# Kernel optimization log

Hardware: AMD Instinct MI355X
Metric: run time of the kernel (lower is better)

## Reference

```python
import jax, jax.numpy as jnp
import numpy as np

LN_EPS = 1e-5


def setup_inputs() -> dict:
    key = jax.random.key(0)
    k1, k2 = jax.random.split(key, 2)
    B, N, D = 8, 4096, 1024
    Z = jax.random.normal(k1, (B, N, D), dtype=jnp.float32)
    # raw decay parameter (sigmoid is applied in forward, as in the torch module)
    decay = jnp.float32(0.9)
    # nn.Linear(d, d): weight [D, D] (out, in), bias [D]
    W = jax.random.normal(k2, (D, D), dtype=jnp.float32) / np.sqrt(D).astype(np.float32)
    b = jnp.zeros((D,), dtype=jnp.float32)
    # nn.LayerNorm(d): gamma/beta
    gamma = jnp.ones((D,), dtype=jnp.float32)
    beta = jnp.zeros((D,), dtype=jnp.float32)
    return {"Z": Z, "decay": decay, "W": W, "b": b, "gamma": gamma, "beta": beta}


def _ema_scan(Z, a):
    """s_t = a * s_{t-1} + Z_t via O(log N) associative scan over slot axis."""
    B, N, D = Z.shape
    A = jnp.full((B, N, 1), a, dtype=Z.dtype)  # broadcast decay coeff per step

    def combine(x, y):
        a1, b1 = x
        a2, b2 = y
        return (a1 * a2, b1 * a2 + b2)

    _, S = jax.lax.associative_scan(combine, (A, Z), axis=1)
    return S  # [B, N, D]


def reference(Z, decay, W, b, gamma, beta):
    a = jax.nn.sigmoid(decay)
    S = _ema_scan(Z, a)                                  # EMA state per slot
    Y = jnp.einsum('bnd,ed->bne', S, W) + b              # per-step Linear, batched
    mu = jnp.mean(Y, axis=-1, keepdims=True)             # LayerNorm over D
    var = jnp.mean((Y - mu) ** 2, axis=-1, keepdims=True)
    Yn = (Y - mu) * jax.lax.rsqrt(var + LN_EPS)
    return Yn * gamma + beta
```

## Files before the change

kernel.cpp:

```cpp
#include <hip/hip_runtime.h>
#include <hip/hip_bf16.h>
#include <cstdint>
#include <cstddef>

#define NB 8
#define NN 4096
#define ND 1024
#define NM (NB*NN)
#define CH 64
#define NCHK (NN/CH)
#define WU 32
#define LN_EPS 1e-5f

typedef __bf16 bf16x8 __attribute__((ext_vector_type(8)));
typedef float  f32x4  __attribute__((ext_vector_type(4)));

typedef __attribute__((address_space(1))) unsigned int guint;
typedef __attribute__((address_space(3))) unsigned int luint;

__device__ __forceinline__ float sigmoidf_(float x) { return 1.f / (1.f + __expf(-x)); }

__device__ __forceinline__ unsigned short f2bf(float x) {
  __hip_bfloat16 h = __float2bfloat16(x);
  return *reinterpret_cast<unsigned short*>(&h);
}
__device__ __forceinline__ float bf2f(unsigned short u) {
  unsigned int v = ((unsigned int)u) << 16;
  return *reinterpret_cast<float*>(&v);
}

__global__ void scan_conv(const float* __restrict__ Z, const float* __restrict__ decay,
                          unsigned short* __restrict__ Sl,
                          const float* __restrict__ W, unsigned short* __restrict__ Wb) {
  const int bid = (int)blockIdx.x;
  if (bid >= NB * NCHK) {
    const int i = (bid - NB * NCHK) * 256 + (int)threadIdx.x;
    float4 v = reinterpret_cast<const float4*>(W)[i];
    ushort4 o;
    o.x = f2bf(v.x); o.y = f2bf(v.y); o.z = f2bf(v.z); o.w = f2bf(v.w);
    reinterpret_cast<ushort4*>(Wb)[i] = o;
    return;
  }
  const float a = sigmoidf_(decay[0]);
  const int c  = bid & (NCHK - 1);
  const int d4 = (int)threadIdx.x;
  const float4* zc = reinterpret_cast<const float4*>(Z + (size_t)bid * CH * ND) + d4;
  ushort4* so = reinterpret_cast<ushort4*>(Sl + (size_t)bid * CH * ND) + d4;
  float4 s = {0.f, 0.f, 0.f, 0.f};
  if (c != 0) {
    const float4* zw = zc - (size_t)WU * (ND / 4);
#pragma unroll 4
    for (int j = 0; j < WU; ++j) {
      float4 v = zw[(size_t)j * (ND / 4)];
      s.x = fmaf(a, s.x, v.x);
      s.y = fmaf(a, s.y, v.y);
      s.z = fmaf(a, s.z, v.z);
      s.w = fmaf(a, s.w, v.w);
    }
  }
#pragma unroll 4
  for (int j = 0; j < CH; ++j) {
    float4 v = zc[(size_t)j * (ND / 4)];
    s.x = fmaf(a, s.x, v.x);
    s.y = fmaf(a, s.y, v.y);
    s.z = fmaf(a, s.z, v.z);
    s.w = fmaf(a, s.w, v.w);
    ushort4 o;
    o.x = f2bf(s.x); o.y = f2bf(s.y); o.z = f2bf(s.z); o.w = f2bf(s.w);
    so[(size_t)j * (ND / 4)] = o;
  }
}

#define BAR()    asm volatile("s_barrier" ::: "memory")
#define LGKM0()  asm volatile("s_waitcnt lgkmcnt(0)" ::: "memory")
#define VM6()    asm volatile("s_waitcnt vmcnt(6)" ::: "memory")
#define VM0()    asm volatile("s_waitcnt vmcnt(0)" ::: "memory")
#define SCHED0() __builtin_amdgcn_sched_barrier(0)
#define PRIO1    __builtin_amdgcn_s_setprio(1)
#define PRIO0    __builtin_amdgcn_s_setprio(0)

#define LOAD_A(qm, D) _Pragma("unroll") for (int i = 0; i < 4; ++i) { \
    aF[i][0] = *(const bf16x8*)(smem + (D)*65536 + aBase + ((qm)*64 + i*16)*128 + swz0); \
    aF[i][1] = *(const bf16x8*)(smem + (D)*65536 + aBase + ((qm)*64 + i*16)*128 + swz1); }

#define LOAD_B(qn, D) _Pragma("unroll") for (int fc = 0; fc < 2; ++fc) { \
    bF[qn][fc][0] = *(const bf16x8*)(smem + (D)*65536 + bBase + ((qn)*32 + fc*16)*128 + swz0); \
    bF[qn][fc][1] = *(const bf16x8*)(smem + (D)*65536 + bBase + ((qn)*32 + fc*16)*128 + swz1); }

#define MFMA_Q(qm, qn) _Pragma("unroll") for (int i = 0; i < 4; ++i) \
    _Pragma("unroll") for (int fc = 0; fc < 2; ++fc) { \
    acc[(qm)*4+i][(qn)*2+fc] = __builtin_amdgcn_mfma_f32_16x16x32_bf16(aF[i][0], bF[qn][fc][0], acc[(qm)*4+i][(qn)*2+fc], 0, 0, 0); \
    acc[(qm)*4+i][(qn)*2+fc] = __builtin_amdgcn_mfma_f32_16x16x32_bf16(aF[i][1], bF[qn][fc][1], acc[(qm)*4+i][(qn)*2+fc], 0, 0, 0); }

#define TILE(t, D, STA, STB, STC, DOVM6, DOVM0) do { \
    LOAD_A(0, D); LOAD_B(0, D); \
    if (STA) stage_h(4*(t)+7); \
    BAR(); LGKM0(); SCHED0(); \
    PRIO1; MFMA_Q(0, 0); PRIO0; SCHED0(); BAR(); \
    LOAD_B(1, D); \
    BAR(); LGKM0(); SCHED0(); \
    PRIO1; MFMA_Q(0, 1); PRIO0; SCHED0(); BAR(); \
    LOAD_A(1, D); \
    if (STB) { stage_h(4*(t)+8); stage_h(4*(t)+9); } \
    BAR(); LGKM0(); SCHED0(); \
    PRIO1; MFMA_Q(1, 0); PRIO0; SCHED0(); BAR(); \
    if (STC) stage_h(4*(t)+10); \
    if (DOVM6) VM6(); \
    if (DOVM0) VM0(); \
    BAR(); \
    PRIO1; MFMA_Q(1, 1); PRIO0; SCHED0(); BAR(); \
  } while (0)

__global__ void __launch_bounds__(512, 2) gemm256(
    const unsigned short* __restrict__ A,
    const unsigned short* __restrict__ Bm,
    const float* __restrict__ bias,
    unsigned short* __restrict__ Yb) {
  extern __shared__ char smem[];
  const int tid  = (int)threadIdx.x;
  const int wid  = tid >> 6, lane = tid & 63;
  const int wr   = wid >> 2, wc = wid & 3;
  const int r16  = lane & 15, kg = lane >> 4;

  const int L = (int)blockIdx.x;
  const int G = (L & 7) * 64 + (L >> 3);
  const int bmAbs = (G >> 2) * 256;
  const int bnAbs = (G & 3) * 256;

  auto stage_h = [&](int h) {
    const int s = h >> 2, j = h & 3;
    const int isB = (j >> 1) ^ 1;
    const int half = j & 1;
    const unsigned short* base = isB ? Bm : A;
    const int rowAbs = (isB ? bnAbs : bmAbs) + half * 128 + wid * 16 + (lane >> 3);
    const int col = s * 64 + (((lane & 7) ^ (lane >> 3)) << 3);
    const int ldsOff = ((s & 1) << 16) + (isB << 15) + (half << 14) + (wid << 11);
    __builtin_amdgcn_global_load_lds((const guint*)(base + (size_t)rowAbs * ND + col),
                                     (luint*)(smem + ldsOff), 16, 0, 0);
    __builtin_amdgcn_global_load_lds((const guint*)(base + (size_t)(rowAbs + 8) * ND + col),
                                     (luint*)(smem + ldsOff + 1024), 16, 0, 0);
  };

  bf16x8 aF[4][2];
  bf16x8 bF[2][2][2];
  f32x4 acc[8][4];
  const f32x4 z4 = {0.f, 0.f, 0.f, 0.f};
#pragma unroll
  for (int m = 0; m < 8; ++m)
#pragma unroll
    for (int n = 0; n < 4; ++n) acc[m][n] = z4;

  const int aBase = (wr << 14) + r16 * 128;
  const int bBase = (1 << 15) + ((wc >> 1) << 14) + (((wc & 1) << 6) + r16) * 128;
  const int swz0 = ((kg)     ^ (lane & 7)) << 4;
  const int swz1 = ((4 + kg) ^ (lane & 7)) << 4;

#pragma unroll
  for (int h = 0; h < 7; ++h) stage_h(h);
  VM6(); BAR();

#pragma unroll 1
  for (int it = 0; it < 7; ++it) {
    TILE(2 * it,     0, 1, 1, 1, 1, 0);
    TILE(2 * it + 1, 1, 1, 1, 1, 1, 0);
  }
  TILE(14, 0, 1, 0, 0, 0, 1);
  TILE(15, 1, 0, 0, 0, 0, 0);

  float bv[4];
#pragma unroll
  for (int n = 0; n < 4; ++n) bv[n] = bias[bnAbs + wc * 64 + n * 16 + r16];
#pragma unroll
  for (int m = 0; m < 8; ++m) {
    const int row0 = wr * 128 + m * 16 + kg * 4;
#pragma unroll
    for (int n = 0; n < 4; ++n) {
      const int col = wc * 64 + n * 16 + r16;
#pragma unroll
      for (int r = 0; r < 4; ++r)
        *reinterpret_cast<unsigned short*>(smem + (row0 + r) * 512 + col * 2) =
            f2bf(acc[m][n][r] + bv[n]);
    }
  }
  __syncthreads();
#pragma unroll
  for (int i = 0; i < 16; ++i) {
    const int idx = i * 512 + tid;
    const int row = idx >> 5;
    const int c16 = idx & 31;
    uint4 v = *reinterpret_cast<const uint4*>(smem + idx * 16);
    *reinterpret_cast<uint4*>(Yb + (size_t)(bmAbs + row) * ND + bnAbs + c16 * 8) = v;
  }
}

__global__ void lnorm(const unsigned short* __restrict__ Yb, float* __restrict__ out,
                      const float* __restrict__ gamma, const float* __restrict__ beta) {
  const int w = threadIdx.x >> 6;
  const int l = threadIdx.x & 63;
  const size_t row = (size_t)blockIdx.x * 4 + w;
  const ushort4* yb = reinterpret_cast<const ushort4*>(Yb + row * ND);
  float* y = out + row * ND;

  float4 v[4];
  float s = 0.f, s2 = 0.f;
#pragma unroll
  for (int i = 0; i < 4; ++i) {
    ushort4 u = yb[i * 64 + l];
    v[i].x = bf2f(u.x); v[i].y = bf2f(u.y); v[i].z = bf2f(u.z); v[i].w = bf2f(u.w);
    s  += v[i].x + v[i].y + v[i].z + v[i].w;
    s2 += v[i].x * v[i].x + v[i].y * v[i].y + v[i].z * v[i].z + v[i].w * v[i].w;
  }
#pragma unroll
  for (int off = 32; off > 0; off >>= 1) {
    s  += __shfl_xor(s, off);
    s2 += __shfl_xor(s2, off);
  }
  const float mean = s * (1.f / ND);
  const float var  = s2 * (1.f / ND) - mean * mean;
  const float rstd = rsqrtf(var + LN_EPS);
#pragma unroll
  for (int i = 0; i < 4; ++i) {
    float4 g  = reinterpret_cast<const float4*>(gamma)[i * 64 + l];
    float4 bt = reinterpret_cast<const float4*>(beta)[i * 64 + l];
    float4 o;
    o.x = (v[i].x - mean) * rstd * g.x + bt.x;
    o.y = (v[i].y - mean) * rstd * g.y + bt.y;
    o.z = (v[i].z - mean) * rstd * g.z + bt.z;
    o.w = (v[i].w - mean) * rstd * g.w + bt.w;
    reinterpret_cast<float4*>(y)[i * 64 + l] = o;
  }
}

extern "C" void kernel_launch(void* const* d_in, const int* in_sizes, int n_in,
                              void* d_out, int out_size, void* d_ws, size_t ws_size,
                              hipStream_t stream) {
  const float* Z     = (const float*)d_in[0];
  const float* decay = (const float*)d_in[1];
  const float* W     = (const float*)d_in[2];
  const float* bias  = (const float*)d_in[3];
  const float* gamma = (const float*)d_in[4];
  const float* beta  = (const float*)d_in[5];
  float* out = (float*)d_out;

  char* ws = (char*)d_ws;
  unsigned short* Sl = (unsigned short*)ws;
  unsigned short* Wb = (unsigned short*)(ws + 67108864);
  unsigned short* Yb = (unsigned short*)(ws + 69206016);

  (void)hipFuncSetAttribute((const void*)gemm256,
                            hipFuncAttributeMaxDynamicSharedMemorySize, 131072);

  scan_conv<<<NB * NCHK + 1024, 256, 0, stream>>>(Z, decay, Sl, W, Wb);
  gemm256<<<512, 512, 131072, stream>>>(Sl, Wb, bias, Yb);
  lnorm<<<8192, 256, 0, stream>>>(Yb, out, gamma, beta);

  (void)in_sizes; (void)n_in; (void)out_size; (void)ws_size;
}
```

Before: 342.8 us.

## Software-pipeline LDS fragment loads across MFMA quadrants with cross-tile prefetch

Restructures the GEMM main loop so LDS fragment reads for the next quadrant (and the next tile's first A/B fragments) are issued before the current MFMA block. Partial lgkmcnt waits replace full drains, and several barriers are removed, so LDS latency can overlap with MFMA work. A second A-fragment register set is added and launch bounds drop to one block per SM to allow the extra registers. The trade-off is that occupancy may fall and the reduced barriers raise the risk of LDS read/write hazards with the double-buffered staging.

```diff
diff --git a/kernel.cpp b/kernel.cpp
--- a/kernel.cpp
+++ b/kernel.cpp
@@ -72,46 +72,58 @@
 }
 
 #define BAR()    asm volatile("s_barrier" ::: "memory")
-#define LGKM0()  asm volatile("s_waitcnt lgkmcnt(0)" ::: "memory")
+#define LGKMC(n) asm volatile("s_waitcnt lgkmcnt(" #n ")" ::: "memory")
 #define VM6()    asm volatile("s_waitcnt vmcnt(6)" ::: "memory")
 #define VM0()    asm volatile("s_waitcnt vmcnt(0)" ::: "memory")
 #define SCHED0() __builtin_amdgcn_sched_barrier(0)
 #define PRIO1    __builtin_amdgcn_s_setprio(1)
 #define PRIO0    __builtin_amdgcn_s_setprio(0)
 
-#define LOAD_A(qm, D) _Pragma("unroll") for (int i = 0; i < 4; ++i) { \
-    aF[i][0] = *(const bf16x8*)(smem + (D)*65536 + aBase + ((qm)*64 + i*16)*128 + swz0); \
-    aF[i][1] = *(const bf16x8*)(smem + (D)*65536 + aBase + ((qm)*64 + i*16)*128 + swz1); }
-
-#define LOAD_B(qn, D) _Pragma("unroll") for (int fc = 0; fc < 2; ++fc) { \
-    bF[qn][fc][0] = *(const bf16x8*)(smem + (D)*65536 + bBase + ((qn)*32 + fc*16)*128 + swz0); \
-    bF[qn][fc][1] = *(const bf16x8*)(smem + (D)*65536 + bBase + ((qn)*32 + fc*16)*128 + swz1); }
-
-#define MFMA_Q(qm, qn) _Pragma("unroll") for (int i = 0; i < 4; ++i) \
+#define DSL_A0(D) _Pragma("unroll") for (int i = 0; i < 4; ++i) { \
+    aFa[i][0] = *(const bf16x8*)(smem + (D)*65536 + aBase + (i*16)*128 + swz0); \
+    aFa[i][1] = *(const bf16x8*)(smem + (D)*65536 + aBase + (i*16)*128 + swz1); }
+#define DSL_A1(D) _Pragma("unroll") for (int i = 0; i < 4; ++i) { \
+    aFb[i][0] = *(const bf16x8*)(smem + (D)*65536 + aBase + (64 + i*16)*128 + swz0); \
+    aFb[i][1] = *(const bf16x8*)(smem + (D)*65536 + aBase + (64 + i*16)*128 + swz1); }
+#define DSL_B0(D) _Pragma("unroll") for (int fc = 0; fc < 2; ++fc) { \
+    bF[0][fc][0] = *(const bf16x8*)(smem + (D)*65536 + bBase + (fc*16)*128 + swz0); \
+    bF[0][fc][1] = *(const bf16x8*)(smem + (D)*65536 + bBase + (fc*16)*128 + swz1); }
+#define DSL_B1(D) _Pragma("unroll") for (int fc = 0; fc < 2; ++fc) { \
+    bF[1][fc][0] = *(const bf16x8*)(smem + (D)*65536 + bBase + (32 + fc*16)*128 + swz0); \
+    bF[1][fc][1] = *(const bf16x8*)(smem + (D)*65536 + bBase + (32 + fc*16)*128 + swz1); }
+
+#define MFMA_Q2(AR, qm, qn) _Pragma("unroll") for (int i = 0; i < 4; ++i) \
     _Pragma("unroll") for (int fc = 0; fc < 2; ++fc) { \
-    acc[(qm)*4+i][(qn)*2+fc] = __builtin_amdgcn_mfma_f32_16x16x32_bf16(aF[i][0], bF[qn][fc][0], acc[(qm)*4+i][(qn)*2+fc], 0, 0, 0); \
-    acc[(qm)*4+i][(qn)*2+fc] = __builtin_amdgcn_mfma_f32_16x16x32_bf16(aF[i][1], bF[qn][fc][1], acc[(qm)*4+i][(qn)*2+fc], 0, 0, 0); }
-
-#define TILE(t, D, STA, STB, STC, DOVM6, DOVM0) do { \
-    LOAD_A(0, D); LOAD_B(0, D); \
-    if (STA) stage_h(4*(t)+7); \
-    BAR(); LGKM0(); SCHED0(); \
-    PRIO1; MFMA_Q(0, 0); PRIO0; SCHED0(); BAR(); \
-    LOAD_B(1, D); \
-    BAR(); LGKM0(); SCHED0(); \
-    PRIO1; MFMA_Q(0, 1); PRIO0; SCHED0(); BAR(); \
-    LOAD_A(1, D); \
-    if (STB) { stage_h(4*(t)+8); stage_h(4*(t)+9); } \
-    BAR(); LGKM0(); SCHED0(); \
-    PRIO1; MFMA_Q(1, 0); PRIO0; SCHED0(); BAR(); \
-    if (STC) stage_h(4*(t)+10); \
+    acc[(qm)*4+i][(qn)*2+fc] = __builtin_amdgcn_mfma_f32_16x16x32_bf16(AR[i][0], bF[qn][fc][0], acc[(qm)*4+i][(qn)*2+fc], 0, 0, 0); \
+    acc[(qm)*4+i][(qn)*2+fc] = __builtin_amdgcn_mfma_f32_16x16x32_bf16(AR[i][1], bF[qn][fc][1], acc[(qm)*4+i][(qn)*2+fc], 0, 0, 0); }
+
+#define TILEP(t, D, STA_, STBC_, DOVM6, DOVM0, PREF) do { \
+     \
+    DSL_B1(D); \
+    LGKMC(4); SCHED0(); \
+    PRIO1; MFMA_Q2(aFa, 0, 0); PRIO0; \
+    if (STA_) stage_h(4*(t)+7); \
+    BAR(); \
+     \
+    DSL_A1(D); \
+    LGKMC(8); SCHED0(); \
+    PRIO1; MFMA_Q2(aFa, 0, 1); PRIO0; \
+    BAR(); \
+     \
+    if (STBC_) { stage_h(4*(t)+8); stage_h(4*(t)+9); stage_h(4*(t)+10); } \
+    LGKMC(0); SCHED0(); \
+    PRIO1; MFMA_Q2(aFb, 1, 0); PRIO0; \
     if (DOVM6) VM6(); \
     if (DOVM0) VM0(); \
     BAR(); \
-    PRIO1; MFMA_Q(1, 1); PRIO0; SCHED0(); BAR(); \
+     \
+    if (PREF) { DSL_A0((D)^1); DSL_B0((D)^1); } \
+    SCHED0(); \
+    PRIO1; MFMA_Q2(aFb, 1, 1); PRIO0; \
+    BAR(); \
   } while (0)
 
-__global__ void __launch_bounds__(512, 2) gemm256(
+__global__ void __launch_bounds__(512, 1) gemm256(
     const unsigned short* __restrict__ A,
     const unsigned short* __restrict__ Bm,
     const float* __restrict__ bias,
@@ -141,7 +153,8 @@
                                      (luint*)(smem + ldsOff + 1024), 16, 0, 0);
   };
 
-  bf16x8 aF[4][2];
+  bf16x8 aFa[4][2];
+  bf16x8 aFb[4][2];
   bf16x8 bF[2][2][2];
   f32x4 acc[8][4];
   const f32x4 z4 = {0.f, 0.f, 0.f, 0.f};
@@ -158,14 +171,15 @@
 #pragma unroll
   for (int h = 0; h < 7; ++h) stage_h(h);
   VM6(); BAR();
+  DSL_A0(0); DSL_B0(0);
 
 #pragma unroll 1
   for (int it = 0; it < 7; ++it) {
-    TILE(2 * it,     0, 1, 1, 1, 1, 0);
-    TILE(2 * it + 1, 1, 1, 1, 1, 1, 0);
-  }
-  TILE(14, 0, 1, 0, 0, 0, 1);
-  TILE(15, 1, 0, 0, 0, 0, 0);
+    TILEP(2 * it,     0, 1, 1, 1, 0, 1);
+    TILEP(2 * it + 1, 1, 1, 1, 1, 0, 1);
+  }
+  TILEP(14, 0, 1, 0, 0, 1, 1);
+  TILEP(15, 1, 0, 0, 0, 0, 0);
 
   float bv[4];
 #pragma unroll
```

New measurement: 372.9 us. 1.09x slower.
